# Performance work log

Hardware: AMD Instinct MI355X
Metric: run time of the kernel (lower is better)

## Reference

```python
import jax, jax.numpy as jnp
import numpy as np

D = 128
TEM_TOTAL = 32
ENT_TOTAL = 1000000
REL_TOTAL = 500
B = 4096
TEM_LEN = 4


def _l2_normalize_rows(w):
    return w / jnp.linalg.norm(w, axis=1, keepdims=True)


def setup_inputs() -> dict:
    key = jax.random.key(0)
    ks = jax.random.split(key, 16)
    inp = {
        "pos_h": jax.random.randint(ks[0], (B,), 0, ENT_TOTAL, dtype=jnp.int32),
        "pos_t": jax.random.randint(ks[1], (B,), 0, ENT_TOTAL, dtype=jnp.int32),
        "pos_r": jax.random.randint(ks[2], (B,), 0, REL_TOTAL, dtype=jnp.int32),
        "pos_tem": jax.random.randint(ks[3], (B, TEM_LEN), 0, TEM_TOTAL, dtype=jnp.int32),
        "neg_h": jax.random.randint(ks[4], (B,), 0, ENT_TOTAL, dtype=jnp.int32),
        "neg_t": jax.random.randint(ks[5], (B,), 0, ENT_TOTAL, dtype=jnp.int32),
        "neg_r": jax.random.randint(ks[6], (B,), 0, REL_TOTAL, dtype=jnp.int32),
        "neg_tem": jax.random.randint(ks[7], (B, TEM_LEN), 0, TEM_TOTAL, dtype=jnp.int32),
    }
    # xavier_uniform then row-wise L2 normalization, as in __init__
    def xavier(k, shape):
        a = float(np.sqrt(6.0 / (shape[0] + shape[1])))
        return jax.random.uniform(k, shape, jnp.float32, -a, a)
    inp["ent_emb"] = _l2_normalize_rows(xavier(ks[8], (ENT_TOTAL, D)))
    inp["rel_emb"] = _l2_normalize_rows(xavier(ks[9], (REL_TOTAL, D)))
    inp["tem_emb"] = _l2_normalize_rows(xavier(ks[10], (TEM_TOTAL, D)))
    # single-layer LSTM params, PyTorch layout: gates ordered (i, f, g, o)
    kk = 1.0 / np.sqrt(D)
    inp["W_ih"] = jax.random.uniform(ks[11], (4 * D, D), jnp.float32, -kk, kk)
    inp["W_hh"] = jax.random.uniform(ks[12], (4 * D, D), jnp.float32, -kk, kk)
    inp["b_ih"] = jax.random.uniform(ks[13], (4 * D,), jnp.float32, -kk, kk)
    inp["b_hh"] = jax.random.uniform(ks[14], (4 * D,), jnp.float32, -kk, kk)
    return inp


def _lstm_last_hidden(x, W_ih, W_hh, b_ih, b_hh):
    # x: [B, T, D] -> final hidden state [B, D] (PyTorch gate order i,f,g,o)
    Bsz, T, d = x.shape
    b = b_ih + b_hh
    xg = jnp.einsum("btd,gd->btg", x, W_ih) + b  # precompute input gates [B,T,4D]

    def step(carry, xt):
        h, c = carry
        gates = xt + h @ W_hh.T
        i, f, g, o = jnp.split(gates, 4, axis=-1)
        i = jax.nn.sigmoid(i)
        f = jax.nn.sigmoid(f)
        g = jnp.tanh(g)
        o = jax.nn.sigmoid(o)
        c = f * c + i * g
        h = o * jnp.tanh(c)
        return (h, c), None

    h0 = jnp.zeros((Bsz, d), x.dtype)
    (h, _), _ = jax.lax.scan(step, (h0, h0), jnp.swapaxes(xg, 0, 1))
    return h


def reference(pos_h, pos_t, pos_r, pos_tem, neg_h, neg_t, neg_r, neg_tem,
              ent_emb, rel_emb, tem_emb, W_ih, W_hh, b_ih, b_hh):
    pos_h_e = ent_emb[pos_h]            # [B, D]
    pos_t_e = ent_emb[pos_t]
    pos_r_e = rel_emb[pos_r]
    tem_e = tem_emb[pos_tem]            # [B, T, D]
    # sequence per sample: [relation_emb, tem_token_embs...] -> [B, 1+T, D]
    seq = jnp.concatenate([pos_r_e[:, None, :], tem_e], axis=1)
    pos_rseq_e = _lstm_last_hidden(seq, W_ih, W_hh, b_ih, b_hh)  # [B, D]

    neg_h_e = ent_emb[neg_h]
    neg_t_e = ent_emb[neg_t]
    # NOTE: original code computes neg sequence embeddings too, but the score
    # uses pos_rseq_e for BOTH pos and neg (as written in the source).
    # L1_flag = True
    pos = jnp.sum(jnp.abs(pos_h_e + pos_rseq_e - pos_t_e), axis=1)
    neg = jnp.sum(jnp.abs(neg_h_e + pos_rseq_e - neg_t_e), axis=1)
    return pos, neg
```

## Files before the change

kernel.cpp:

```cpp
#include <hip/hip_runtime.h>
#include <math.h>

#define D 128
#define G4 512
#define BATCH 4096
#define TEM_LEN 4
#define REL_TOTAL 500
#define TEM_TOTAL 32
#define NSTEP 5
#define BT 16

__device__ __forceinline__ float fsigmoid(float x) {
    return 1.0f / (1.0f + __expf(-x));
}
__device__ __forceinline__ float ftanh(float x) {
    return 1.0f - 2.0f / (__expf(2.0f * x) + 1.0f);
}

__global__ __launch_bounds__(512) void precompute_xg(
    const float* __restrict__ rel_emb, const float* __restrict__ tem_emb,
    const float* __restrict__ W_ih, const float* __restrict__ b_ih,
    const float* __restrict__ b_hh, float* __restrict__ xg)
{
    __shared__ float srow[D];
    const int row = blockIdx.x;
    const float* src = (row < REL_TOTAL) ? (rel_emb + row * D)
                                         : (tem_emb + (row - REL_TOTAL) * D);
    const int tid = threadIdx.x;
    if (tid < D) srow[tid] = src[tid];
    __syncthreads();

    const int g = tid;
    const float4* w = (const float4*)(W_ih + g * D);
    float acc = b_ih[g] + b_hh[g];
#pragma unroll
    for (int j = 0; j < D / 4; ++j) {
        float4 wv = w[j];
        float4 hv = *(const float4*)(&srow[4 * j]);
        acc += wv.x * hv.x + wv.y * hv.y + wv.z * hv.z + wv.w * hv.w;
    }
    xg[row * G4 + g] = acc;
}

__global__ __launch_bounds__(512) void lstm_score(
    const int* __restrict__ pos_h, const int* __restrict__ pos_t,
    const int* __restrict__ pos_r, const int* __restrict__ pos_tem,
    const int* __restrict__ neg_h, const int* __restrict__ neg_t,
    const float* __restrict__ ent_emb, const float* __restrict__ W_hh,
    const float* __restrict__ xg, float* __restrict__ out)
{
    __shared__ float sh[BT][D];
    __shared__ float scell[BT][D];
    __shared__ float sg[BT][G4];
    __shared__ int   soff[NSTEP][BT];

    const int tid = threadIdx.x;
    const int b0 = blockIdx.x * BT;

    if (tid < NSTEP * BT) {
        int t = tid / BT, r = tid % BT;
        int off;
        if (t == 0) off = pos_r[b0 + r] * G4;
        else        off = (REL_TOTAL + pos_tem[(b0 + r) * TEM_LEN + (t - 1)]) * G4;
        soff[t][r] = off;
    }
    for (int i = tid; i < BT * D; i += 512) {
        ((float*)sh)[i] = 0.0f;
        ((float*)scell)[i] = 0.0f;
    }
    __syncthreads();

    const int g = tid;
    const float4* wrow = (const float4*)(W_hh + g * D);

    for (int t = 0; t < NSTEP; ++t) {
        float acc[BT];
#pragma unroll
        for (int r = 0; r < BT; ++r) acc[r] = xg[soff[t][r] + g];

        if (t > 0) {
#pragma unroll
            for (int kc = 0; kc < 4; ++kc) {
                float4 w[8];
#pragma unroll
                for (int j = 0; j < 8; ++j) w[j] = wrow[kc * 8 + j];
#pragma unroll
                for (int r = 0; r < BT; ++r) {
#pragma unroll
                    for (int j = 0; j < 8; ++j) {
                        float4 hv = *(const float4*)(&sh[r][kc * 32 + 4 * j]);
                        acc[r] += w[j].x * hv.x + w[j].y * hv.y
                                + w[j].z * hv.z + w[j].w * hv.w;
                    }
                }
            }
        }
#pragma unroll
        for (int r = 0; r < BT; ++r) sg[r][g] = acc[r];
        __syncthreads();

#pragma unroll
        for (int i = 0; i < 4; ++i) {
            int e = tid + i * 512;
            int r = e >> 7, d = e & (D - 1);
            float xi = sg[r][d];
            float xf = sg[r][D + d];
            float xc = sg[r][2 * D + d];
            float xo = sg[r][3 * D + d];
            float ii = fsigmoid(xi), ff = fsigmoid(xf);
            float gg = ftanh(xc),   oo = fsigmoid(xo);
            float cc = ff * scell[r][d] + ii * gg;
            scell[r][d] = cc;
            sh[r][d] = oo * ftanh(cc);
        }
        __syncthreads();
    }

    const int row  = tid >> 5;
    const int lane = tid & 31;
    const int b    = b0 + row;
    const int d0   = lane * 4;
    float4 hh  = *(const float4*)(&sh[row][d0]);
    float4 phe = *(const float4*)(ent_emb + (long long)pos_h[b] * D + d0);
    float4 pte = *(const float4*)(ent_emb + (long long)pos_t[b] * D + d0);
    float4 nhe = *(const float4*)(ent_emb + (long long)neg_h[b] * D + d0);
    float4 nte = *(const float4*)(ent_emb + (long long)neg_t[b] * D + d0);
    float ps = fabsf(phe.x + hh.x - pte.x) + fabsf(phe.y + hh.y - pte.y)
             + fabsf(phe.z + hh.z - pte.z) + fabsf(phe.w + hh.w - pte.w);
    float ns = fabsf(nhe.x + hh.x - nte.x) + fabsf(nhe.y + hh.y - nte.y)
             + fabsf(nhe.z + hh.z - nte.z) + fabsf(nhe.w + hh.w - nte.w);
#pragma unroll
    for (int off = 16; off >= 1; off >>= 1) {
        ps += __shfl_xor(ps, off, 64);
        ns += __shfl_xor(ns, off, 64);
    }
    if (lane == 0) {
        out[b] = ps;
        out[BATCH + b] = ns;
    }
}

extern "C" void kernel_launch(void* const* d_in, const int* in_sizes, int n_in,
                              void* d_out, int out_size, void* d_ws, size_t ws_size,
                              hipStream_t stream) {
    const int*   pos_h   = (const int*)d_in[0];
    const int*   pos_t   = (const int*)d_in[1];
    const int*   pos_r   = (const int*)d_in[2];
    const int*   pos_tem = (const int*)d_in[3];
    const int*   neg_h   = (const int*)d_in[4];
    const int*   neg_t   = (const int*)d_in[5];
    const float* ent_emb = (const float*)d_in[8];
    const float* rel_emb = (const float*)d_in[9];
    const float* tem_emb = (const float*)d_in[10];
    const float* W_ih    = (const float*)d_in[11];
    const float* W_hh    = (const float*)d_in[12];
    const float* b_ih    = (const float*)d_in[13];
    const float* b_hh    = (const float*)d_in[14];
    float* out = (float*)d_out;
    float* xg  = (float*)d_ws;

    precompute_xg<<<REL_TOTAL + TEM_TOTAL, 512, 0, stream>>>(
        rel_emb, tem_emb, W_ih, b_ih, b_hh, xg);
    lstm_score<<<BATCH / BT, 512, 0, stream>>>(
        pos_h, pos_t, pos_r, pos_tem, neg_h, neg_t, ent_emb, W_hh, xg, out);
}
```

Measured before the change: 663.3 us.

## Restructure LSTM so each thread owns one hidden unit across all four gates

The LSTM kernel now uses 128 threads per block, each owning one hidden dimension and computing all four gate pre-activations for 8 batch rows. The cell state stays in registers, and a double-buffered hidden state in shared memory removes the gate scratch buffer and one barrier per step. The input-gate precompute now does 4 rows per block so each W_ih load is reused. The trade-offs are more blocks with smaller batch tiles, so each W_hh row is reused across fewer samples, and more register pressure from 32 accumulators.

New measurement: 658.9 us. No clear change (-0.7%).

```diff
diff --git a/kernel.cpp b/kernel.cpp
--- a/kernel.cpp
+++ b/kernel.cpp
@@ -7,8 +7,10 @@
 #define TEM_LEN 4
 #define REL_TOTAL 500
 #define TEM_TOTAL 32
+#define NROWS (REL_TOTAL + TEM_TOTAL)
 #define NSTEP 5
-#define BT 16
+#define BT 8
+#define XRPB 4
 
 __device__ __forceinline__ float fsigmoid(float x) {
     return 1.0f / (1.0f + __expf(-x));
@@ -22,36 +24,49 @@
     const float* __restrict__ W_ih, const float* __restrict__ b_ih,
     const float* __restrict__ b_hh, float* __restrict__ xg)
 {
-    __shared__ float srow[D];
-    const int row = blockIdx.x;
-    const float* src = (row < REL_TOTAL) ? (rel_emb + row * D)
-                                         : (tem_emb + (row - REL_TOTAL) * D);
+    __shared__ float srow[XRPB][D];
+    const int r0 = blockIdx.x * XRPB;
     const int tid = threadIdx.x;
-    if (tid < D) srow[tid] = src[tid];
+
+    {
+        int rr = tid >> 7, dd = tid & (D - 1);
+        int row = r0 + rr;
+        const float* src = (row < REL_TOTAL) ? (rel_emb + row * D)
+                                             : (tem_emb + (row - REL_TOTAL) * D);
+        srow[rr][dd] = src[dd];
+    }
     __syncthreads();
 
     const int g = tid;
     const float4* w = (const float4*)(W_ih + g * D);
-    float acc = b_ih[g] + b_hh[g];
+    const float b = b_ih[g] + b_hh[g];
+    float a0 = b, a1 = b, a2 = b, a3 = b;
 #pragma unroll
     for (int j = 0; j < D / 4; ++j) {
         float4 wv = w[j];
-        float4 hv = *(const float4*)(&srow[4 * j]);
-        acc += wv.x * hv.x + wv.y * hv.y + wv.z * hv.z + wv.w * hv.w;
+        float4 h0 = *(const float4*)(&srow[0][4 * j]);
+        float4 h1 = *(const float4*)(&srow[1][4 * j]);
+        float4 h2 = *(const float4*)(&srow[2][4 * j]);
+        float4 h3 = *(const float4*)(&srow[3][4 * j]);
+        a0 += wv.x * h0.x + wv.y * h0.y + wv.z * h0.z + wv.w * h0.w;
+        a1 += wv.x * h1.x + wv.y * h1.y + wv.z * h1.z + wv.w * h1.w;
+        a2 += wv.x * h2.x + wv.y * h2.y + wv.z * h2.z + wv.w * h2.w;
+        a3 += wv.x * h3.x + wv.y * h3.y + wv.z * h3.z + wv.w * h3.w;
     }
-    xg[row * G4 + g] = acc;
+    xg[(r0 + 0) * G4 + g] = a0;
+    xg[(r0 + 1) * G4 + g] = a1;
+    xg[(r0 + 2) * G4 + g] = a2;
+    xg[(r0 + 3) * G4 + g] = a3;
 }
 
-__global__ __launch_bounds__(512) void lstm_score(
+__global__ __launch_bounds__(128) void lstm_score(
     const int* __restrict__ pos_h, const int* __restrict__ pos_t,
     const int* __restrict__ pos_r, const int* __restrict__ pos_tem,
     const int* __restrict__ neg_h, const int* __restrict__ neg_t,
     const float* __restrict__ ent_emb, const float* __restrict__ W_hh,
     const float* __restrict__ xg, float* __restrict__ out)
 {
-    __shared__ float sh[BT][D];
-    __shared__ float scell[BT][D];
-    __shared__ float sg[BT][G4];
+    __shared__ float hbuf[2][BT][D];
     __shared__ int   soff[NSTEP][BT];
 
     const int tid = threadIdx.x;
@@ -59,82 +74,95 @@
 
     if (tid < NSTEP * BT) {
         int t = tid / BT, r = tid % BT;
-        int off;
-        if (t == 0) off = pos_r[b0 + r] * G4;
-        else        off = (REL_TOTAL + pos_tem[(b0 + r) * TEM_LEN + (t - 1)]) * G4;
-        soff[t][r] = off;
-    }
-    for (int i = tid; i < BT * D; i += 512) {
-        ((float*)sh)[i] = 0.0f;
-        ((float*)scell)[i] = 0.0f;
+        soff[t][r] = ((t == 0) ? pos_r[b0 + r]
+                               : (REL_TOTAL + pos_tem[(b0 + r) * TEM_LEN + (t - 1)])) * G4;
     }
     __syncthreads();
 
-    const int g = tid;
-    const float4* wrow = (const float4*)(W_hh + g * D);
+    const int d = tid;
+    float c[BT];
+#pragma unroll
+    for (int r = 0; r < BT; ++r) c[r] = 0.0f;
+
+    const float4* wq0 = (const float4*)(W_hh + (0 * D + d) * D);
+    const float4* wq1 = (const float4*)(W_hh + (1 * D + d) * D);
+    const float4* wq2 = (const float4*)(W_hh + (2 * D + d) * D);
+    const float4* wq3 = (const float4*)(W_hh + (3 * D + d) * D);
 
     for (int t = 0; t < NSTEP; ++t) {
-        float acc[BT];
+        float acc[BT][4];
 #pragma unroll
-        for (int r = 0; r < BT; ++r) acc[r] = xg[soff[t][r] + g];
+        for (int r = 0; r < BT; ++r) {
+            const float* x = xg + soff[t][r] + d;
+            acc[r][0] = x[0];
+            acc[r][1] = x[D];
+            acc[r][2] = x[2 * D];
+            acc[r][3] = x[3 * D];
+        }
 
         if (t > 0) {
+            const float (*hp)[D] = hbuf[(t - 1) & 1];
+            for (int kc = 0; kc < 8; ++kc) {
+                float4 w0[4], w1[4], w2[4], w3[4];
 #pragma unroll
-            for (int kc = 0; kc < 4; ++kc) {
-                float4 w[8];
-#pragma unroll
-                for (int j = 0; j < 8; ++j) w[j] = wrow[kc * 8 + j];
+                for (int j = 0; j < 4; ++j) {
+                    w0[j] = wq0[kc * 4 + j];
+                    w1[j] = wq1[kc * 4 + j];
+                    w2[j] = wq2[kc * 4 + j];
+                    w3[j] = wq3[kc * 4 + j];
+                }
 #pragma unroll
                 for (int r = 0; r < BT; ++r) {
 #pragma unroll
-                    for (int j = 0; j < 8; ++j) {
-                        float4 hv = *(const float4*)(&sh[r][kc * 32 + 4 * j]);
-                        acc[r] += w[j].x * hv.x + w[j].y * hv.y
-                                + w[j].z * hv.z + w[j].w * hv.w;
+                    for (int j = 0; j < 4; ++j) {
+                        float4 hv = *(const float4*)(&hp[r][kc * 16 + 4 * j]);
+                        acc[r][0] += w0[j].x * hv.x + w0[j].y * hv.y + w0[j].z * hv.z + w0[j].w * hv.w;
+                        acc[r][1] += w1[j].x * hv.x + w1[j].y * hv.y + w1[j].z * hv.z + w1[j].w * hv.w;
+                        acc[r][2] += w2[j].x * hv.x + w2[j].y * hv.y + w2[j].z * hv.z + w2[j].w * hv.w;
+                        acc[r][3] += w3[j].x * hv.x + w3[j].y * hv.y + w3[j].z * hv.z + w3[j].w * hv.w;
                     }
                 }
             }
         }
-#pragma unroll
-        for (int r = 0; r < BT; ++r) sg[r][g] = acc[r];
-        __syncthreads();
 
 #pragma unroll
-        for (int i = 0; i < 4; ++i) {
-            int e = tid + i * 512;
-            int r = e >> 7, d = e & (D - 1);
-            float xi = sg[r][d];
-            float xf = sg[r][D + d];
-            float xc = sg[r][2 * D + d];
-            float xo = sg[r][3 * D + d];
-            float ii = fsigmoid(xi), ff = fsigmoid(xf);
-            float gg = ftanh(xc),   oo = fsigmoid(xo);
-            float cc = ff * scell[r][d] + ii * gg;
-            scell[r][d] = cc;
-            sh[r][d] = oo * ftanh(cc);
+        for (int r = 0; r < BT; ++r) {
+            float ii = fsigmoid(acc[r][0]);
+            float ff = fsigmoid(acc[r][1]);
+            float gg = ftanh(acc[r][2]);
+            float oo = fsigmoid(acc[r][3]);
+            float cc = ff * c[r] + ii * gg;
+            c[r] = cc;
+            hbuf[t & 1][r][d] = oo * ftanh(cc);
         }
         __syncthreads();
     }
 
-    const int row  = tid >> 5;
-    const int lane = tid & 31;
-    const int b    = b0 + row;
-    const int d0   = lane * 4;
-    float4 hh  = *(const float4*)(&sh[row][d0]);
-    float4 phe = *(const float4*)(ent_emb + (long long)pos_h[b] * D + d0);
-    float4 pte = *(const float4*)(ent_emb + (long long)pos_t[b] * D + d0);
-    float4 nhe = *(const float4*)(ent_emb + (long long)neg_h[b] * D + d0);
-    float4 nte = *(const float4*)(ent_emb + (long long)neg_t[b] * D + d0);
-    float ps = fabsf(phe.x + hh.x - pte.x) + fabsf(phe.y + hh.y - pte.y)
-             + fabsf(phe.z + hh.z - pte.z) + fabsf(phe.w + hh.w - pte.w);
-    float ns = fabsf(nhe.x + hh.x - nte.x) + fabsf(nhe.y + hh.y - nte.y)
-             + fabsf(nhe.z + hh.z - nte.z) + fabsf(nhe.w + hh.w - nte.w);
+    const float (*hf)[D] = hbuf[(NSTEP - 1) & 1];
+    const int r  = tid >> 4;
+    const int s  = tid & 15;
+    const int b  = b0 + r;
+    const int d0 = s * 8;
+    const float4* ph = (const float4*)(ent_emb + (size_t)pos_h[b] * D + d0);
+    const float4* pt = (const float4*)(ent_emb + (size_t)pos_t[b] * D + d0);
+    const float4* nh = (const float4*)(ent_emb + (size_t)neg_h[b] * D + d0);
+    const float4* nt = (const float4*)(ent_emb + (size_t)neg_t[b] * D + d0);
+    float ps = 0.0f, ns = 0.0f;
 #pragma unroll
-    for (int off = 16; off >= 1; off >>= 1) {
+    for (int u = 0; u < 2; ++u) {
+        float4 hh = *(const float4*)(&hf[r][d0 + 4 * u]);
+        float4 a = ph[u], bb = pt[u], cg = nh[u], dd = nt[u];
+        ps += fabsf(a.x + hh.x - bb.x) + fabsf(a.y + hh.y - bb.y)
+            + fabsf(a.z + hh.z - bb.z) + fabsf(a.w + hh.w - bb.w);
+        ns += fabsf(cg.x + hh.x - dd.x) + fabsf(cg.y + hh.y - dd.y)
+            + fabsf(cg.z + hh.z - dd.z) + fabsf(cg.w + hh.w - dd.w);
+    }
+#pragma unroll
+    for (int off = 8; off >= 1; off >>= 1) {
         ps += __shfl_xor(ps, off, 64);
         ns += __shfl_xor(ns, off, 64);
     }
-    if (lane == 0) {
+    if (s == 0) {
         out[b] = ps;
         out[BATCH + b] = ns;
     }
@@ -159,8 +187,8 @@
     float* out = (float*)d_out;
     float* xg  = (float*)d_ws;
 
-    precompute_xg<<<REL_TOTAL + TEM_TOTAL, 512, 0, stream>>>(
+    precompute_xg<<<NROWS / XRPB, 512, 0, stream>>>(
         rel_emb, tem_emb, W_ih, b_ih, b_hh, xg);
-    lstm_score<<<BATCH / BT, 512, 0, stream>>>(
+    lstm_score<<<BATCH / BT, 128, 0, stream>>>(
         pos_h, pos_t, pos_r, pos_tem, neg_h, neg_t, ent_emb, W_hh, xg, out);
 }
```
